# Optimization experiments

Measured on AMD Instinct MI355X. Metric: run time of the kernel, lower is better.

## Reference

```python
import jax, jax.numpy as jnp
import numpy as np


def conv1d(x, w, b, pad):
    # x: (B, Cin, T), w: (Cout, Cin, K), b: (Cout,)
    y = jax.lax.conv_general_dilated(x, w, window_strides=(1,), padding=[(pad, pad)],
                                     dimension_numbers=('NCH', 'OIH', 'NCH'))
    return y + b[None, :, None]


def setup_inputs() -> dict:
    key = jax.random.key(0)
    ks = jax.random.split(key, 16)
    B, Cmel, Ctxt, Catt, T1, T2 = 16, 80, 256, 80, 800, 200
    s = 0.05
    return {
        'queries': jax.random.normal(ks[0], (B, Cmel, T1), jnp.float32),
        'keys': jax.random.normal(ks[1], (B, Ctxt, T2), jnp.float32),
        'attn_prior': jax.random.uniform(ks[2], (B, T1, T2), jnp.float32),
        # key_proj: Conv1d(256->512,k=3,pad=1) -> ReLU -> Conv1d(512->80,k=1)
        'kw1': jax.random.normal(ks[3], (Ctxt * 2, Ctxt, 3), jnp.float32) * s,
        'kb1': jax.random.normal(ks[4], (Ctxt * 2,), jnp.float32) * s,
        'kw2': jax.random.normal(ks[5], (Catt, Ctxt * 2, 1), jnp.float32) * s,
        'kb2': jax.random.normal(ks[6], (Catt,), jnp.float32) * s,
        # query_proj (3xconv): 80->160 k3 -> ReLU -> 160->80 k1 -> ReLU -> 80->80 k1
        'qw1': jax.random.normal(ks[7], (Cmel * 2, Cmel, 3), jnp.float32) * s,
        'qb1': jax.random.normal(ks[8], (Cmel * 2,), jnp.float32) * s,
        'qw2': jax.random.normal(ks[9], (Cmel, Cmel * 2, 1), jnp.float32) * s,
        'qb2': jax.random.normal(ks[10], (Cmel,), jnp.float32) * s,
        'qw3': jax.random.normal(ks[11], (Catt, Cmel, 1), jnp.float32) * s,
        'qb3': jax.random.normal(ks[12], (Catt,), jnp.float32) * s,
    }


def reference(queries, keys, attn_prior, kw1, kb1, kw2, kb2, qw1, qb1, qw2, qb2, qw3, qb3):
    # key encoder
    k = jax.nn.relu(conv1d(keys, kw1, kb1, pad=1))
    k = conv1d(k, kw2, kb2, pad=0)                      # (B, Catt, T2)
    # query encoder ('3xconv')
    q = jax.nn.relu(conv1d(queries, qw1, qb1, pad=1))
    q = jax.nn.relu(conv1d(q, qw2, qb2, pad=0))
    q = conv1d(q, qw3, qb3, pad=0)                      # (B, Catt, T1)
    # L2 distance over channels: ||q||^2 + ||k||^2 - 2 q.k (same math as broadcast (q-k)^2 sum)
    q2 = jnp.sum(q * q, axis=1)                         # (B, T1)
    k2 = jnp.sum(k * k, axis=1)                         # (B, T2)
    qk = jnp.einsum('bct,bcs->bts', q, k)               # (B, T1, T2)
    attn = -0.0005 * (q2[:, :, None] + k2[:, None, :] - 2.0 * qk)[:, None]  # (B,1,T1,T2)
    attn = jax.nn.log_softmax(attn, axis=3) + jnp.log(attn_prior[:, None] + 1e-8)
    return attn
```

## Files before the change

### kernel.cpp

```cpp
#include <hip/hip_runtime.h>
#include <cstdint>
#include <cmath>

using short8  = __attribute__((ext_vector_type(8))) short;
using short4v = __attribute__((ext_vector_type(4))) short;
using floatx4 = __attribute__((ext_vector_type(4))) float;

__device__ __forceinline__ short f2bf(float f) {
  union { float f; unsigned u; } x; x.f = f;
  unsigned r = x.u + 0x7FFFu + ((x.u >> 16) & 1u);
  return (short)(r >> 16);
}

__global__ __launch_bounds__(256) void prep_kernel(
    const float* __restrict__ keys, const float* __restrict__ queries,
    const float* __restrict__ kw1, const float* __restrict__ kw2,
    const float* __restrict__ qw1, const float* __restrict__ qw2,
    const float* __restrict__ qw3,
    short* __restrict__ kT0, short* __restrict__ qT0,
    short* __restrict__ w1, short* __restrict__ w2, short* __restrict__ w3,
    short* __restrict__ w4, short* __restrict__ w5)
{
  const int bid = blockIdx.x, tid = threadIdx.x;
  __shared__ float xs[32][65];

  if (bid < 1136) {
    const float* src; short* dst; int CIN, T, CP, bx, by, b;
    if (bid < 512) {
      src = keys; dst = kT0; CIN = 256; T = 200; CP = 256;
      bx = bid & 3; by = (bid >> 2) & 7; b = bid >> 5;
    } else {
      int b2 = bid - 512;
      src = queries; dst = qT0; CIN = 80; T = 800; CP = 96;
      bx = b2 % 13; by = (b2 / 13) % 3; b = b2 / 39;
    }
    const int t0 = bx * 64, ci0 = by * 32;
    for (int i = tid; i < 32 * 64; i += 256) {
      int row = i >> 6, col = i & 63;
      float v = 0.f;
      if (ci0 + row < CIN && t0 + col < T)
        v = src[((size_t)b * CIN + ci0 + row) * T + t0 + col];
      xs[row][col] = v;
    }
    __syncthreads();
    int t = tid >> 2, c8 = (tid & 3) * 8;
    if (t0 + t < T) {
      short8 o;
      #pragma unroll
      for (int j = 0; j < 8; ++j) o[j] = f2bf(xs[c8 + j][t]);
      *(short8*)&dst[((size_t)b * T + t0 + t) * CP + ci0 + c8] = o;
    }
  } else {
    int blk = bid - 1136;
    const float* src; short* dst; int base, tot;
    int CoP, CiP, Cout, CIN, K;
    if      (blk < 384) { src=kw1; dst=w1; base=0;   CoP=512; CiP=256; Cout=512; CIN=256; K=3; }
    else if (blk < 432) { src=kw2; dst=w2; base=384; CoP=96;  CiP=512; Cout=80;  CIN=512; K=1; }
    else if (blk < 486) { src=qw1; dst=w3; base=432; CoP=192; CiP=96;  Cout=160; CIN=80;  K=3; }
    else if (blk < 504) { src=qw2; dst=w4; base=486; CoP=96;  CiP=192; Cout=80;  CIN=160; K=1; }
    else                { src=qw3; dst=w5; base=504; CoP=96;  CiP=96;  Cout=80;  CIN=80;  K=1; }
    tot = K * CoP * CiP;
    int b0 = (blk - base) * 1024;
    for (int e = 0; e < 4; ++e) {
      int gi = b0 + e * 256 + tid;
      if (gi < tot) {
        int dk  = gi / (CoP * CiP);
        int rem = gi - dk * (CoP * CiP);
        int co  = rem / CiP, ci = rem - (rem / CiP) * CiP;
        float v = (co < Cout && ci < CIN) ? src[((size_t)co * CIN + ci) * K + dk] : 0.f;
        dst[gi] = f2bf(v);
      }
    }
  }
}

__global__ __launch_bounds__(256) void encoders_kernel(
    const short* __restrict__ kT0, const short* __restrict__ qT0,
    const short* __restrict__ w1, const short* __restrict__ w2,
    const short* __restrict__ w3, const short* __restrict__ w4,
    const short* __restrict__ w5,
    const float* __restrict__ kb1, const float* __restrict__ kb2,
    const float* __restrict__ qb1, const float* __restrict__ qb2,
    const float* __restrict__ qb3,
    short* __restrict__ kF, short* __restrict__ qF)
{
  __shared__ __align__(16) short smem[25680];
  const int tid = threadIdx.x, wid = tid >> 6, lane = tid & 63;
  const int q = lane >> 4, m = lane & 15;
  short* xs = smem;

  if (blockIdx.x < 64) {
    const int b = blockIdx.x >> 2, t0 = (blockIdx.x & 3) * 64;
    short* y1c = smem + 2640;

    floatx4 acc2[6];
    #pragma unroll
    for (int f = 0; f < 6; ++f) acc2[f] = (floatx4){0.f, 0.f, 0.f, 0.f};

    for (int half = 0; half < 2; ++half) {
      floatx4 acc1[4][4];
      #pragma unroll
      for (int f = 0; f < 4; ++f)
        #pragma unroll
        for (int tf = 0; tf < 4; ++tf) acc1[f][tf] = (floatx4){0.f, 0.f, 0.f, 0.f};

      for (int c0 = 0; c0 < 8; ++c0) {
        __syncthreads();
        for (int i = tid; i < 66 * 4; i += 256) {
          int row = i >> 2, c8 = (i & 3) * 8;
          int t = t0 + row - 1;
          int4 v = {0, 0, 0, 0};
          if (t >= 0 && t < 200)
            v = *(const int4*)&kT0[((size_t)b * 200 + t) * 256 + c0 * 32 + c8];
          *(int4*)&xs[row * 40 + c8] = v;
        }
        __syncthreads();
        #pragma unroll
        for (int dk = 0; dk < 3; ++dk) {
          short8 fa[4];
          #pragma unroll
          for (int f = 0; f < 4; ++f)
            fa[f] = *(const short8*)&w1[((size_t)(dk * 512 + half * 256 + wid * 64 + f * 16 + m)) * 256
                                        + c0 * 32 + q * 8];
          #pragma unroll
          for (int tf = 0; tf < 4; ++tf) {
            short8 fb = *(const short8*)&xs[(tf * 16 + m + dk) * 40 + q * 8];
            #pragma unroll
            for (int f = 0; f < 4; ++f)
              acc1[f][tf] = __builtin_amdgcn_mfma_f32_16x16x32_bf16(fa[f], fb, acc1[f][tf], 0, 0, 0);
          }
        }
      }
      __syncthreads();
      #pragma unroll
      for (int f = 0; f < 4; ++f) {
        #pragma unroll
        for (int tf = 0; tf < 4; ++tf) {
          int co_l = wid * 64 + f * 16 + q * 4;
          int co   = half * 256 + co_l;
          int t    = tf * 16 + m;
          short4v o;
          #pragma unroll
          for (int r = 0; r < 4; ++r)
            o[r] = f2bf(fmaxf(acc1[f][tf][r] + kb1[co + r], 0.f));
          *(short4v*)&y1c[(co_l >> 5) * 2560 + t * 40 + (co_l & 31)] = o;
        }
      }
      __syncthreads();
      #pragma unroll
      for (int c = 0; c < 8; ++c) {
        short8 fb = *(const short8*)&y1c[c * 2560 + (wid * 16 + m) * 40 + q * 8];
        #pragma unroll
        for (int f = 0; f < 6; ++f) {
          short8 fa = *(const short8*)&w2[((size_t)(f * 16 + m)) * 512 + half * 256 + c * 32 + q * 8];
          acc2[f] = __builtin_amdgcn_mfma_f32_16x16x32_bf16(fa, fb, acc2[f], 0, 0, 0);
        }
      }
    }
    int t = t0 + wid * 16 + m;
    if (t < 200) {
      #pragma unroll
      for (int f = 0; f < 6; ++f) {
        int co = f * 16 + q * 4;
        short4v o;
        #pragma unroll
        for (int r = 0; r < 4; ++r) {
          float bv = (co + r < 80) ? kb2[co + r] : 0.f;
          o[r] = f2bf(acc2[f][r] + bv);
        }
        *(short4v*)&kF[((size_t)b * 200 + t) * 96 + co] = o;
      }
    }
  } else {
    const int qbid = blockIdx.x - 64;
    const int b = qbid / 13, t0 = (qbid % 13) * 64;
    short* y1c = smem + 2640;
    short* y2c = smem + 18000;

    floatx4 accq[3][4];
    #pragma unroll
    for (int f = 0; f < 3; ++f)
      #pragma unroll
      for (int tf = 0; tf < 4; ++tf) accq[f][tf] = (floatx4){0.f, 0.f, 0.f, 0.f};

    for (int c0 = 0; c0 < 3; ++c0) {
      __syncthreads();
      for (int i = tid; i < 66 * 4; i += 256) {
        int row = i >> 2, c8 = (i & 3) * 8;
        int t = t0 + row - 1;
        int4 v = {0, 0, 0, 0};
        if (t >= 0 && t < 800)
          v = *(const int4*)&qT0[((size_t)b * 800 + t) * 96 + c0 * 32 + c8];
        *(int4*)&xs[row * 40 + c8] = v;
      }
      __syncthreads();
      #pragma unroll
      for (int dk = 0; dk < 3; ++dk) {
        short8 fa[3];
        #pragma unroll
        for (int f = 0; f < 3; ++f)
          fa[f] = *(const short8*)&w3[((size_t)(dk * 192 + wid * 48 + f * 16 + m)) * 96
                                      + c0 * 32 + q * 8];
        #pragma unroll
        for (int tf = 0; tf < 4; ++tf) {
          short8 fb = *(const short8*)&xs[(tf * 16 + m + dk) * 40 + q * 8];
          #pragma unroll
          for (int f = 0; f < 3; ++f)
            accq[f][tf] = __builtin_amdgcn_mfma_f32_16x16x32_bf16(fa[f], fb, accq[f][tf], 0, 0, 0);
        }
      }
    }
    __syncthreads();
    #pragma unroll
    for (int f = 0; f < 3; ++f) {
      #pragma unroll
      for (int tf = 0; tf < 4; ++tf) {
        int co = wid * 48 + f * 16 + q * 4;
        int t  = tf * 16 + m;
        short4v o;
        #pragma unroll
        for (int r = 0; r < 4; ++r) {
          float bv = (co + r < 160) ? qb1[co + r] : 0.f;
          o[r] = f2bf(fmaxf(accq[f][tf][r] + bv, 0.f));
        }
        *(short4v*)&y1c[(co >> 5) * 2560 + t * 40 + (co & 31)] = o;
      }
    }
    __syncthreads();

    floatx4 acc2q[6];
    #pragma unroll
    for (int f = 0; f < 6; ++f) acc2q[f] = (floatx4){0.f, 0.f, 0.f, 0.f};
    #pragma unroll
    for (int c = 0; c < 6; ++c) {
      short8 fb = *(const short8*)&y1c[c * 2560 + (wid * 16 + m) * 40 + q * 8];
      #pragma unroll
      for (int f = 0; f < 6; ++f) {
        short8 fa = *(const short8*)&w4[((size_t)(f * 16 + m)) * 192 + c * 32 + q * 8];
        acc2q[f] = __builtin_amdgcn_mfma_f32_16x16x32_bf16(fa, fb, acc2q[f], 0, 0, 0);
      }
    }
    #pragma unroll
    for (int f = 0; f < 6; ++f) {
      int co = f * 16 + q * 4;
      int t  = wid * 16 + m;
      short4v o;
      #pragma unroll
      for (int r = 0; r < 4; ++r) {
        float bv = (co + r < 80) ? qb2[co + r] : 0.f;
        o[r] = f2bf(fmaxf(acc2q[f][r] + bv, 0.f));
      }
      *(short4v*)&y2c[(co >> 5) * 2560 + t * 40 + (co & 31)] = o;
    }
    __syncthreads();

    floatx4 acc3q[6];
    #pragma unroll
    for (int f = 0; f < 6; ++f) acc3q[f] = (floatx4){0.f, 0.f, 0.f, 0.f};
    #pragma unroll
    for (int c = 0; c < 3; ++c) {
      short8 fb = *(const short8*)&y2c[c * 2560 + (wid * 16 + m) * 40 + q * 8];
      #pragma unroll
      for (int f = 0; f < 6; ++f) {
        short8 fa = *(const short8*)&w5[((size_t)(f * 16 + m)) * 96 + c * 32 + q * 8];
        acc3q[f] = __builtin_amdgcn_mfma_f32_16x16x32_bf16(fa, fb, acc3q[f], 0, 0, 0);
      }
    }
    int t = t0 + wid * 16 + m;
    if (t < 800) {
      #pragma unroll
      for (int f = 0; f < 6; ++f) {
        int co = f * 16 + q * 4;
        short4v o;
        #pragma unroll
        for (int r = 0; r < 4; ++r) {
          float bv = (co + r < 80) ? qb3[co + r] : 0.f;
          o[r] = f2bf(acc3q[f][r] + bv);
        }
        *(short4v*)&qF[((size_t)b * 800 + t) * 96 + co] = o;
      }
    }
  }
}

__global__ __launch_bounds__(256) void attn_mfma(
    const short* __restrict__ qT, const short* __restrict__ kT,
    const float* __restrict__ prior, float* __restrict__ out)
{
  const int b = blockIdx.y, t1_0 = blockIdx.x * 64;
  const int tid = threadIdx.x, wid = tid >> 6, lane = tid & 63;
  const int q = lane >> 4, m = lane & 15;

  __shared__ __align__(16) short aq[64 * 104];
  __shared__ __align__(16) short bk[208 * 40];
  __shared__ float k2s[208];

  floatx4 acc[13];
  #pragma unroll
  for (int f = 0; f < 13; ++f) acc[f] = (floatx4){0.f, 0.f, 0.f, 0.f};

  for (int i = tid; i < 64 * 12; i += 256) {
    int row = i / 12, g = i - (i / 12) * 12;
    int4 v = {0, 0, 0, 0};
    if (t1_0 + row < 800)
      v = *(const int4*)&qT[((size_t)b * 800 + t1_0 + row) * 96 + g * 8];
    *(int4*)&aq[row * 104 + g * 8] = v;
  }

  float k2acc = 0.f;
  for (int c = 0; c < 3; ++c) {
    __syncthreads();
    for (int i = tid; i < 208 * 4; i += 256) {
      int row = i >> 2, g = i & 3;
      int4 v = {0, 0, 0, 0};
      if (row < 200)
        v = *(const int4*)&kT[((size_t)b * 200 + row) * 96 + c * 32 + g * 8];
      *(int4*)&bk[row * 40 + g * 8] = v;
    }
    __syncthreads();
    if (tid < 208) {
      #pragma unroll
      for (int g = 0; g < 4; ++g) {
        short8 s = *(const short8*)&bk[tid * 40 + g * 8];
        #pragma unroll
        for (int j = 0; j < 8; ++j) {
          union { unsigned u; float f; } x; x.u = ((unsigned)(unsigned short)s[j]) << 16;
          k2acc = fmaf(x.f, x.f, k2acc);
        }
      }
    }
    short8 fa = *(const short8*)&aq[(wid * 16 + m) * 104 + c * 32 + q * 8];
    #pragma unroll
    for (int f = 0; f < 13; ++f) {
      short8 fb = *(const short8*)&bk[(f * 16 + m) * 40 + q * 8];
      acc[f] = __builtin_amdgcn_mfma_f32_16x16x32_bf16(fa, fb, acc[f], 0, 0, 0);
    }
  }
  if (tid < 208) k2s[tid] = k2acc;
  __syncthreads();

  float k2v[13];
  #pragma unroll
  for (int f = 0; f < 13; ++f) k2v[f] = k2s[f * 16 + m];

  float mx[4] = {-INFINITY, -INFINITY, -INFINITY, -INFINITY};
  #pragma unroll
  for (int f = 0; f < 13; ++f) {
    bool valid = (f * 16 + m) < 200;
    #pragma unroll
    for (int r = 0; r < 4; ++r) {
      float v = valid ? (0.001f * acc[f][r] - 0.0005f * k2v[f]) : -INFINITY;
      acc[f][r] = v;
      mx[r] = fmaxf(mx[r], v);
    }
  }
  #pragma unroll
  for (int msk = 1; msk < 16; msk <<= 1)
    #pragma unroll
    for (int r = 0; r < 4; ++r) mx[r] = fmaxf(mx[r], __shfl_xor(mx[r], msk));
  float sm[4] = {0.f, 0.f, 0.f, 0.f};
  #pragma unroll
  for (int f = 0; f < 13; ++f)
    #pragma unroll
    for (int r = 0; r < 4; ++r) sm[r] += __expf(acc[f][r] - mx[r]);
  #pragma unroll
  for (int msk = 1; msk < 16; msk <<= 1)
    #pragma unroll
    for (int r = 0; r < 4; ++r) sm[r] += __shfl_xor(sm[r], msk);
  float lse[4];
  #pragma unroll
  for (int r = 0; r < 4; ++r) lse[r] = mx[r] + __logf(sm[r]);

  #pragma unroll
  for (int f = 0; f < 13; ++f) {
    int col = f * 16 + m;
    if (col < 200) {
      #pragma unroll
      for (int r = 0; r < 4; ++r) {
        int t1 = t1_0 + wid * 16 + q * 4 + r;
        if (t1 < 800) {
          size_t o = ((size_t)b * 800 + t1) * 200 + col;
          out[o] = acc[f][r] - lse[r] + __logf(prior[o] + 1e-8f);
        }
      }
    }
  }
}

extern "C" void kernel_launch(void* const* d_in, const int* in_sizes, int n_in,
                              void* d_out, int out_size, void* d_ws, size_t ws_size,
                              hipStream_t stream) {
  const float* queries = (const float*)d_in[0];
  const float* keys    = (const float*)d_in[1];
  const float* prior   = (const float*)d_in[2];
  const float* kw1 = (const float*)d_in[3];
  const float* kb1 = (const float*)d_in[4];
  const float* kw2 = (const float*)d_in[5];
  const float* kb2 = (const float*)d_in[6];
  const float* qw1 = (const float*)d_in[7];
  const float* qb1 = (const float*)d_in[8];
  const float* qw2 = (const float*)d_in[9];
  const float* qb2 = (const float*)d_in[10];
  const float* qw3 = (const float*)d_in[11];
  const float* qb3 = (const float*)d_in[12];
  float* out = (float*)d_out;

  short* p = (short*)d_ws;
  short* kT0 = p;  p += (size_t)3200 * 256;
  short* qT0 = p;  p += (size_t)12800 * 96;
  short* w1  = p;  p += (size_t)3 * 512 * 256;
  short* w2  = p;  p += (size_t)96 * 512;
  short* w3  = p;  p += (size_t)3 * 192 * 96;
  short* w4  = p;  p += (size_t)96 * 192;
  short* w5  = p;  p += (size_t)96 * 96;
  short* kF  = p;  p += (size_t)3200 * 96;
  short* qF  = p;  p += (size_t)12800 * 96;

  prep_kernel<<<dim3(1649), 256, 0, stream>>>(keys, queries, kw1, kw2, qw1, qw2, qw3,
                                              kT0, qT0, w1, w2, w3, w4, w5);
  encoders_kernel<<<dim3(272), 256, 0, stream>>>(kT0, qT0, w1, w2, w3, w4, w5,
                                                 kb1, kb2, qb1, qb2, qb3, kF, qF);
  attn_mfma<<<dim3(13, 16), 256, 0, stream>>>(qF, kF, prior, out);
}
```

Baseline: 169.5 us.

## Split fused key encoder into parallel k3 conv blocks plus separate 1x1 conv kernel

The key-encoder path previously ran on only 64 blocks, each computing all 512 conv1 output channels and then the 1x1 conv, which serialized heavy MFMA work on few CUs. It is now split so that 512 blocks each compute a 64-channel by 64-time tile of the k=3 conv, with weights staged in LDS. The intermediate is written to a new global bf16 buffer, and a separate 64-block kernel performs the 512->80 projection. This trades extra global traffic and a kernel launch for far more parallelism across the GPU.

```diff
diff --git a/kernel.cpp b/kernel.cpp
--- a/kernel.cpp
+++ b/kernel.cpp
@@ -52,14 +52,14 @@
     }
   } else {
     int blk = bid - 1136;
-    const float* src; short* dst; int base, tot;
+    const float* src; short* dst; int base;
     int CoP, CiP, Cout, CIN, K;
     if      (blk < 384) { src=kw1; dst=w1; base=0;   CoP=512; CiP=256; Cout=512; CIN=256; K=3; }
     else if (blk < 432) { src=kw2; dst=w2; base=384; CoP=96;  CiP=512; Cout=80;  CIN=512; K=1; }
     else if (blk < 486) { src=qw1; dst=w3; base=432; CoP=192; CiP=96;  Cout=160; CIN=80;  K=3; }
     else if (blk < 504) { src=qw2; dst=w4; base=486; CoP=96;  CiP=192; Cout=80;  CIN=160; K=1; }
     else                { src=qw3; dst=w5; base=504; CoP=96;  CiP=96;  Cout=80;  CIN=80;  K=1; }
-    tot = K * CoP * CiP;
+    int tot = K * CoP * CiP;
     int b0 = (blk - base) * 1024;
     for (int e = 0; e < 4; ++e) {
       int gi = b0 + e * 256 + tid;
@@ -74,105 +74,77 @@
   }
 }
 
-__global__ __launch_bounds__(256) void encoders_kernel(
+__global__ __launch_bounds__(256) void conv_k3_kernel(
     const short* __restrict__ kT0, const short* __restrict__ qT0,
-    const short* __restrict__ w1, const short* __restrict__ w2,
-    const short* __restrict__ w3, const short* __restrict__ w4,
-    const short* __restrict__ w5,
-    const float* __restrict__ kb1, const float* __restrict__ kb2,
-    const float* __restrict__ qb1, const float* __restrict__ qb2,
-    const float* __restrict__ qb3,
-    short* __restrict__ kF, short* __restrict__ qF)
+    const short* __restrict__ w1, const short* __restrict__ w3,
+    const short* __restrict__ w4, const short* __restrict__ w5,
+    const float* __restrict__ kb1, const float* __restrict__ qb1,
+    const float* __restrict__ qb2, const float* __restrict__ qb3,
+    short* __restrict__ kT1, short* __restrict__ qF)
 {
   __shared__ __align__(16) short smem[25680];
   const int tid = threadIdx.x, wid = tid >> 6, lane = tid & 63;
   const int q = lane >> 4, m = lane & 15;
   short* xs = smem;
 
-  if (blockIdx.x < 64) {
-    const int b = blockIdx.x >> 2, t0 = (blockIdx.x & 3) * 64;
-    short* y1c = smem + 2640;
-
-    floatx4 acc2[6];
-    #pragma unroll
-    for (int f = 0; f < 6; ++f) acc2[f] = (floatx4){0.f, 0.f, 0.f, 0.f};
-
-    for (int half = 0; half < 2; ++half) {
-      floatx4 acc1[4][4];
-      #pragma unroll
-      for (int f = 0; f < 4; ++f)
-        #pragma unroll
-        for (int tf = 0; tf < 4; ++tf) acc1[f][tf] = (floatx4){0.f, 0.f, 0.f, 0.f};
-
-      for (int c0 = 0; c0 < 8; ++c0) {
-        __syncthreads();
-        for (int i = tid; i < 66 * 4; i += 256) {
-          int row = i >> 2, c8 = (i & 3) * 8;
-          int t = t0 + row - 1;
-          int4 v = {0, 0, 0, 0};
-          if (t >= 0 && t < 200)
-            v = *(const int4*)&kT0[((size_t)b * 200 + t) * 256 + c0 * 32 + c8];
-          *(int4*)&xs[row * 40 + c8] = v;
-        }
-        __syncthreads();
-        #pragma unroll
-        for (int dk = 0; dk < 3; ++dk) {
-          short8 fa[4];
-          #pragma unroll
-          for (int f = 0; f < 4; ++f)
-            fa[f] = *(const short8*)&w1[((size_t)(dk * 512 + half * 256 + wid * 64 + f * 16 + m)) * 256
-                                        + c0 * 32 + q * 8];
-          #pragma unroll
-          for (int tf = 0; tf < 4; ++tf) {
-            short8 fb = *(const short8*)&xs[(tf * 16 + m + dk) * 40 + q * 8];
-            #pragma unroll
-            for (int f = 0; f < 4; ++f)
-              acc1[f][tf] = __builtin_amdgcn_mfma_f32_16x16x32_bf16(fa[f], fb, acc1[f][tf], 0, 0, 0);
+  if (blockIdx.x < 512) {
+    const int blk = blockIdx.x;
+    const int b = blk >> 5, co0 = ((blk >> 2) & 7) * 64, t0 = (blk & 3) * 64;
+    const int wy = wid >> 1, wx = wid & 1;
+    short* as = smem + 2640;
+
+    floatx4 acc[2][2];
+    #pragma unroll
+    for (int i = 0; i < 2; ++i)
+      #pragma unroll
+      for (int j = 0; j < 2; ++j) acc[i][j] = (floatx4){0.f, 0.f, 0.f, 0.f};
+
+    for (int c0 = 0; c0 < 8; ++c0) {
+      __syncthreads();
+      for (int i = tid; i < 66 * 4; i += 256) {
+        int row = i >> 2, c8 = (i & 3) * 8;
+        int t = t0 + row - 1;
+        int4 v = {0, 0, 0, 0};
+        if (t >= 0 && t < 200)
+          v = *(const int4*)&kT0[((size_t)b * 200 + t) * 256 + c0 * 32 + c8];
+        *(int4*)&xs[row * 40 + c8] = v;
+      }
+      for (int i = tid; i < 192 * 4; i += 256) {
+        int row = i >> 2, c8 = (i & 3) * 8;
+        int dk = row >> 6, co = row & 63;
+        *(int4*)&as[row * 40 + c8] =
+            *(const int4*)&w1[((size_t)(dk * 512 + co0 + co)) * 256 + c0 * 32 + c8];
+      }
+      __syncthreads();
+      #pragma unroll
+      for (int dk = 0; dk < 3; ++dk) {
+        short8 fa0 = *(const short8*)&as[(dk * 64 + wy * 32 + m) * 40 + q * 8];
+        short8 fa1 = *(const short8*)&as[(dk * 64 + wy * 32 + 16 + m) * 40 + q * 8];
+        #pragma unroll
+        for (int j = 0; j < 2; ++j) {
+          short8 fb = *(const short8*)&xs[(wx * 32 + j * 16 + m + dk) * 40 + q * 8];
+          acc[0][j] = __builtin_amdgcn_mfma_f32_16x16x32_bf16(fa0, fb, acc[0][j], 0, 0, 0);
+          acc[1][j] = __builtin_amdgcn_mfma_f32_16x16x32_bf16(fa1, fb, acc[1][j], 0, 0, 0);
+        }
+      }
+    }
+    #pragma unroll
+    for (int i = 0; i < 2; ++i) {
+      #pragma unroll
+      for (int j = 0; j < 2; ++j) {
+        #pragma unroll
+        for (int r = 0; r < 4; ++r) {
+          int co = co0 + wy * 32 + i * 16 + q * 4 + r;
+          int t  = t0 + wx * 32 + j * 16 + m;
+          if (t < 200) {
+            float v = fmaxf(acc[i][j][r] + kb1[co], 0.f);
+            kT1[((size_t)b * 200 + t) * 512 + co] = f2bf(v);
           }
         }
       }
-      __syncthreads();
-      #pragma unroll
-      for (int f = 0; f < 4; ++f) {
-        #pragma unroll
-        for (int tf = 0; tf < 4; ++tf) {
-          int co_l = wid * 64 + f * 16 + q * 4;
-          int co   = half * 256 + co_l;
-          int t    = tf * 16 + m;
-          short4v o;
-          #pragma unroll
-          for (int r = 0; r < 4; ++r)
-            o[r] = f2bf(fmaxf(acc1[f][tf][r] + kb1[co + r], 0.f));
-          *(short4v*)&y1c[(co_l >> 5) * 2560 + t * 40 + (co_l & 31)] = o;
-        }
-      }
-      __syncthreads();
-      #pragma unroll
-      for (int c = 0; c < 8; ++c) {
-        short8 fb = *(const short8*)&y1c[c * 2560 + (wid * 16 + m) * 40 + q * 8];
-        #pragma unroll
-        for (int f = 0; f < 6; ++f) {
-          short8 fa = *(const short8*)&w2[((size_t)(f * 16 + m)) * 512 + half * 256 + c * 32 + q * 8];
-          acc2[f] = __builtin_amdgcn_mfma_f32_16x16x32_bf16(fa, fb, acc2[f], 0, 0, 0);
-        }
-      }
-    }
-    int t = t0 + wid * 16 + m;
-    if (t < 200) {
-      #pragma unroll
-      for (int f = 0; f < 6; ++f) {
-        int co = f * 16 + q * 4;
-        short4v o;
-        #pragma unroll
-        for (int r = 0; r < 4; ++r) {
-          float bv = (co + r < 80) ? kb2[co + r] : 0.f;
-          o[r] = f2bf(acc2[f][r] + bv);
-        }
-        *(short4v*)&kF[((size_t)b * 200 + t) * 96 + co] = o;
-      }
     }
   } else {
-    const int qbid = blockIdx.x - 64;
+    const int qbid = blockIdx.x - 512;
     const int b = qbid / 13, t0 = (qbid % 13) * 64;
     short* y1c = smem + 2640;
     short* y2c = smem + 18000;
@@ -279,6 +251,47 @@
         }
         *(short4v*)&qF[((size_t)b * 800 + t) * 96 + co] = o;
       }
+    }
+  }
+}
+
+__global__ __launch_bounds__(256) void kconv2_kernel(
+    const short* __restrict__ kT1, const short* __restrict__ w2,
+    const float* __restrict__ kb2, short* __restrict__ kF)
+{
+  const int blk = blockIdx.x;
+  const int b = blk >> 2, t0 = (blk & 3) * 64;
+  const int tid = threadIdx.x, wid = tid >> 6, lane = tid & 63;
+  const int q = lane >> 4, m = lane & 15;
+  const int t = t0 + wid * 16 + m;
+  const bool tv = (t < 200);
+
+  floatx4 acc[6];
+  #pragma unroll
+  for (int f = 0; f < 6; ++f) acc[f] = (floatx4){0.f, 0.f, 0.f, 0.f};
+
+  #pragma unroll
+  for (int c = 0; c < 16; ++c) {
+    short8 fb;
+    if (tv) fb = *(const short8*)&kT1[((size_t)b * 200 + t) * 512 + c * 32 + q * 8];
+    else    fb = (short8){0,0,0,0,0,0,0,0};
+    #pragma unroll
+    for (int f = 0; f < 6; ++f) {
+      short8 fa = *(const short8*)&w2[((size_t)(f * 16 + m)) * 512 + c * 32 + q * 8];
+      acc[f] = __builtin_amdgcn_mfma_f32_16x16x32_bf16(fa, fb, acc[f], 0, 0, 0);
+    }
+  }
+  if (tv) {
+    #pragma unroll
+    for (int f = 0; f < 6; ++f) {
+      int co = f * 16 + q * 4;
+      short4v o;
+      #pragma unroll
+      for (int r = 0; r < 4; ++r) {
+        float bv = (co + r < 80) ? kb2[co + r] : 0.f;
+        o[r] = f2bf(acc[f][r] + bv);
+      }
+      *(short4v*)&kF[((size_t)b * 200 + t) * 96 + co] = o;
     }
   }
 }
@@ -413,12 +426,14 @@
   short* w3  = p;  p += (size_t)3 * 192 * 96;
   short* w4  = p;  p += (size_t)96 * 192;
   short* w5  = p;  p += (size_t)96 * 96;
+  short* kT1 = p;  p += (size_t)3200 * 512;
   short* kF  = p;  p += (size_t)3200 * 96;
   short* qF  = p;  p += (size_t)12800 * 96;
 
   prep_kernel<<<dim3(1649), 256, 0, stream>>>(keys, queries, kw1, kw2, qw1, qw2, qw3,
                                               kT0, qT0, w1, w2, w3, w4, w5);
-  encoders_kernel<<<dim3(272), 256, 0, stream>>>(kT0, qT0, w1, w2, w3, w4, w5,
-                                                 kb1, kb2, qb1, qb2, qb3, kF, qF);
+  conv_k3_kernel<<<dim3(720), 256, 0, stream>>>(kT0, qT0, w1, w3, w4, w5,
+                                                kb1, qb1, qb2, qb3, kT1, qF);
+  kconv2_kernel<<<dim3(64), 256, 0, stream>>>(kT1, w2, kb2, kF);
   attn_mfma<<<dim3(13, 16), 256, 0, stream>>>(qF, kF, prior, out);
 }
```

Measured after the change: 152.7 us. 1.11x faster.

## Fuse input transpose/bf16 conversion into encoders and retile key encoder

Applied to the files above, without the earlier changes.

Removes the separate activation transpose-and-convert pass from the prep kernel; the encoder kernel now reads fp32 keys/queries directly, converts them to bf16 into shared memory, and loads the whole channel range once instead of per channel chunk. The key encoder is retiled to 16 timesteps per block over all 512 output channels (208 blocks instead of 64), which raises parallelism but re-reads the conv weights per block. The attention kernel now stages all key channels at once and computes k² in a single pass, cutting the barriers inside its loop. Uncoalesced strided global reads of fp32 inputs during staging are a possible cost.

```diff
diff --git a/kernel.cpp b/kernel.cpp
--- a/kernel.cpp
+++ b/kernel.cpp
@@ -13,69 +13,36 @@
 }
 
 __global__ __launch_bounds__(256) void prep_kernel(
-    const float* __restrict__ keys, const float* __restrict__ queries,
     const float* __restrict__ kw1, const float* __restrict__ kw2,
     const float* __restrict__ qw1, const float* __restrict__ qw2,
     const float* __restrict__ qw3,
-    short* __restrict__ kT0, short* __restrict__ qT0,
     short* __restrict__ w1, short* __restrict__ w2, short* __restrict__ w3,
     short* __restrict__ w4, short* __restrict__ w5)
 {
-  const int bid = blockIdx.x, tid = threadIdx.x;
-  __shared__ float xs[32][65];
-
-  if (bid < 1136) {
-    const float* src; short* dst; int CIN, T, CP, bx, by, b;
-    if (bid < 512) {
-      src = keys; dst = kT0; CIN = 256; T = 200; CP = 256;
-      bx = bid & 3; by = (bid >> 2) & 7; b = bid >> 5;
-    } else {
-      int b2 = bid - 512;
-      src = queries; dst = qT0; CIN = 80; T = 800; CP = 96;
-      bx = b2 % 13; by = (b2 / 13) % 3; b = b2 / 39;
-    }
-    const int t0 = bx * 64, ci0 = by * 32;
-    for (int i = tid; i < 32 * 64; i += 256) {
-      int row = i >> 6, col = i & 63;
-      float v = 0.f;
-      if (ci0 + row < CIN && t0 + col < T)
-        v = src[((size_t)b * CIN + ci0 + row) * T + t0 + col];
-      xs[row][col] = v;
-    }
-    __syncthreads();
-    int t = tid >> 2, c8 = (tid & 3) * 8;
-    if (t0 + t < T) {
-      short8 o;
-      #pragma unroll
-      for (int j = 0; j < 8; ++j) o[j] = f2bf(xs[c8 + j][t]);
-      *(short8*)&dst[((size_t)b * T + t0 + t) * CP + ci0 + c8] = o;
-    }
-  } else {
-    int blk = bid - 1136;
-    const float* src; short* dst; int base, tot;
-    int CoP, CiP, Cout, CIN, K;
-    if      (blk < 384) { src=kw1; dst=w1; base=0;   CoP=512; CiP=256; Cout=512; CIN=256; K=3; }
-    else if (blk < 432) { src=kw2; dst=w2; base=384; CoP=96;  CiP=512; Cout=80;  CIN=512; K=1; }
-    else if (blk < 486) { src=qw1; dst=w3; base=432; CoP=192; CiP=96;  Cout=160; CIN=80;  K=3; }
-    else if (blk < 504) { src=qw2; dst=w4; base=486; CoP=96;  CiP=192; Cout=80;  CIN=160; K=1; }
-    else                { src=qw3; dst=w5; base=504; CoP=96;  CiP=96;  Cout=80;  CIN=80;  K=1; }
-    tot = K * CoP * CiP;
-    int b0 = (blk - base) * 1024;
-    for (int e = 0; e < 4; ++e) {
-      int gi = b0 + e * 256 + tid;
-      if (gi < tot) {
-        int dk  = gi / (CoP * CiP);
-        int rem = gi - dk * (CoP * CiP);
-        int co  = rem / CiP, ci = rem - (rem / CiP) * CiP;
-        float v = (co < Cout && ci < CIN) ? src[((size_t)co * CIN + ci) * K + dk] : 0.f;
-        dst[gi] = f2bf(v);
-      }
+  const int blk = blockIdx.x, tid = threadIdx.x;
+  const float* src; short* dst; int base;
+  int CoP, CiP, Cout, CIN, K;
+  if      (blk < 384) { src=kw1; dst=w1; base=0;   CoP=512; CiP=256; Cout=512; CIN=256; K=3; }
+  else if (blk < 432) { src=kw2; dst=w2; base=384; CoP=96;  CiP=512; Cout=80;  CIN=512; K=1; }
+  else if (blk < 486) { src=qw1; dst=w3; base=432; CoP=192; CiP=96;  Cout=160; CIN=80;  K=3; }
+  else if (blk < 504) { src=qw2; dst=w4; base=486; CoP=96;  CiP=192; Cout=80;  CIN=160; K=1; }
+  else                { src=qw3; dst=w5; base=504; CoP=96;  CiP=96;  Cout=80;  CIN=80;  K=1; }
+  int tot = K * CoP * CiP;
+  int b0 = (blk - base) * 1024;
+  for (int e = 0; e < 4; ++e) {
+    int gi = b0 + e * 256 + tid;
+    if (gi < tot) {
+      int dk  = gi / (CoP * CiP);
+      int rem = gi - dk * (CoP * CiP);
+      int co  = rem / CiP, ci = rem - (rem / CiP) * CiP;
+      float v = (co < Cout && ci < CIN) ? src[((size_t)co * CIN + ci) * K + dk] : 0.f;
+      dst[gi] = f2bf(v);
     }
   }
 }
 
 __global__ __launch_bounds__(256) void encoders_kernel(
-    const short* __restrict__ kT0, const short* __restrict__ qT0,
+    const float* __restrict__ keys, const float* __restrict__ queries,
     const short* __restrict__ w1, const short* __restrict__ w2,
     const short* __restrict__ w3, const short* __restrict__ w4,
     const short* __restrict__ w5,
@@ -84,98 +51,100 @@
     const float* __restrict__ qb3,
     short* __restrict__ kF, short* __restrict__ qF)
 {
-  __shared__ __align__(16) short smem[25680];
-  const int tid = threadIdx.x, wid = tid >> 6, lane = tid & 63;
+  __shared__ __align__(16) short smem[22224];
+  const int tid = threadIdx.x, wv = tid >> 6, lane = tid & 63;
   const int q = lane >> 4, m = lane & 15;
-  short* xs = smem;
-
-  if (blockIdx.x < 64) {
-    const int b = blockIdx.x >> 2, t0 = (blockIdx.x & 3) * 64;
-    short* y1c = smem + 2640;
-
-    floatx4 acc2[6];
-    #pragma unroll
-    for (int f = 0; f < 6; ++f) acc2[f] = (floatx4){0.f, 0.f, 0.f, 0.f};
-
-    for (int half = 0; half < 2; ++half) {
-      floatx4 acc1[4][4];
-      #pragma unroll
-      for (int f = 0; f < 4; ++f)
-        #pragma unroll
-        for (int tf = 0; tf < 4; ++tf) acc1[f][tf] = (floatx4){0.f, 0.f, 0.f, 0.f};
-
-      for (int c0 = 0; c0 < 8; ++c0) {
-        __syncthreads();
-        for (int i = tid; i < 66 * 4; i += 256) {
-          int row = i >> 2, c8 = (i & 3) * 8;
-          int t = t0 + row - 1;
-          int4 v = {0, 0, 0, 0};
-          if (t >= 0 && t < 200)
-            v = *(const int4*)&kT0[((size_t)b * 200 + t) * 256 + c0 * 32 + c8];
-          *(int4*)&xs[row * 40 + c8] = v;
-        }
-        __syncthreads();
-        #pragma unroll
-        for (int dk = 0; dk < 3; ++dk) {
-          short8 fa[4];
-          #pragma unroll
-          for (int f = 0; f < 4; ++f)
-            fa[f] = *(const short8*)&w1[((size_t)(dk * 512 + half * 256 + wid * 64 + f * 16 + m)) * 256
-                                        + c0 * 32 + q * 8];
-          #pragma unroll
-          for (int tf = 0; tf < 4; ++tf) {
-            short8 fb = *(const short8*)&xs[(tf * 16 + m + dk) * 40 + q * 8];
-            #pragma unroll
-            for (int f = 0; f < 4; ++f)
-              acc1[f][tf] = __builtin_amdgcn_mfma_f32_16x16x32_bf16(fa[f], fb, acc1[f][tf], 0, 0, 0);
-          }
-        }
-      }
-      __syncthreads();
-      #pragma unroll
-      for (int f = 0; f < 4; ++f) {
-        #pragma unroll
-        for (int tf = 0; tf < 4; ++tf) {
-          int co_l = wid * 64 + f * 16 + q * 4;
-          int co   = half * 256 + co_l;
-          int t    = tf * 16 + m;
-          short4v o;
-          #pragma unroll
-          for (int r = 0; r < 4; ++r)
-            o[r] = f2bf(fmaxf(acc1[f][tf][r] + kb1[co + r], 0.f));
-          *(short4v*)&y1c[(co_l >> 5) * 2560 + t * 40 + (co_l & 31)] = o;
-        }
-      }
-      __syncthreads();
-      #pragma unroll
-      for (int c = 0; c < 8; ++c) {
-        short8 fb = *(const short8*)&y1c[c * 2560 + (wid * 16 + m) * 40 + q * 8];
-        #pragma unroll
-        for (int f = 0; f < 6; ++f) {
-          short8 fa = *(const short8*)&w2[((size_t)(f * 16 + m)) * 512 + half * 256 + c * 32 + q * 8];
-          acc2[f] = __builtin_amdgcn_mfma_f32_16x16x32_bf16(fa, fb, acc2[f], 0, 0, 0);
-        }
-      }
-    }
-    int t = t0 + wid * 16 + m;
+
+  if (blockIdx.x < 208) {
+    const int b = blockIdx.x / 13, t0 = (blockIdx.x % 13) * 16;
+    short* xs = smem;
+    short* y1 = smem + 4752;
+
+    {
+      const int ci = tid;
+      #pragma unroll
+      for (int j = 0; j < 18; ++j) {
+        int t = t0 - 1 + j;
+        float v = (t >= 0 && t < 200) ? keys[((size_t)b * 256 + ci) * 200 + t] : 0.f;
+        xs[j * 264 + ci] = f2bf(v);
+      }
+    }
+    __syncthreads();
+
+    floatx4 acc1[8];
+    #pragma unroll
+    for (int f = 0; f < 8; ++f) acc1[f] = (floatx4){0.f, 0.f, 0.f, 0.f};
+
+    for (int c0 = 0; c0 < 8; ++c0) {
+      #pragma unroll
+      for (int dk = 0; dk < 3; ++dk) {
+        short8 fb = *(const short8*)&xs[(m + dk) * 264 + c0 * 32 + q * 8];
+        #pragma unroll
+        for (int f = 0; f < 8; ++f) {
+          short8 fa = *(const short8*)&w1[(size_t)dk * 131072
+                                          + (wv * 128 + f * 16 + m) * 256 + c0 * 32 + q * 8];
+          acc1[f] = __builtin_amdgcn_mfma_f32_16x16x32_bf16(fa, fb, acc1[f], 0, 0, 0);
+        }
+      }
+    }
+    #pragma unroll
+    for (int f = 0; f < 8; ++f) {
+      int co = wv * 128 + f * 16 + q * 4;
+      floatx4 bv = *(const floatx4*)&kb1[co];
+      short4v o;
+      #pragma unroll
+      for (int r = 0; r < 4; ++r) o[r] = f2bf(fmaxf(acc1[f][r] + bv[r], 0.f));
+      *(short4v*)&y1[m * 520 + co] = o;
+    }
+    __syncthreads();
+
+    const int nf = (wv < 2) ? 2 : 1;
+    floatx4 acc2[2];
+    acc2[0] = (floatx4){0.f, 0.f, 0.f, 0.f};
+    acc2[1] = (floatx4){0.f, 0.f, 0.f, 0.f};
+    for (int c0 = 0; c0 < 16; ++c0) {
+      short8 fb = *(const short8*)&y1[m * 520 + c0 * 32 + q * 8];
+      short8 fa0 = *(const short8*)&w2[(wv * 16 + m) * 512 + c0 * 32 + q * 8];
+      acc2[0] = __builtin_amdgcn_mfma_f32_16x16x32_bf16(fa0, fb, acc2[0], 0, 0, 0);
+      if (nf == 2) {
+        short8 fa1 = *(const short8*)&w2[((wv + 4) * 16 + m) * 512 + c0 * 32 + q * 8];
+        acc2[1] = __builtin_amdgcn_mfma_f32_16x16x32_bf16(fa1, fb, acc2[1], 0, 0, 0);
+      }
+    }
+    int t = t0 + m;
     if (t < 200) {
-      #pragma unroll
-      for (int f = 0; f < 6; ++f) {
+      for (int e = 0; e < nf; ++e) {
+        int f = wv + e * 4;
         int co = f * 16 + q * 4;
+        floatx4 bv = {0.f, 0.f, 0.f, 0.f};
+        if (co < 80) bv = *(const floatx4*)&kb2[co];
         short4v o;
         #pragma unroll
-        for (int r = 0; r < 4; ++r) {
-          float bv = (co + r < 80) ? kb2[co + r] : 0.f;
-          o[r] = f2bf(acc2[f][r] + bv);
-        }
+        for (int r = 0; r < 4; ++r) o[r] = f2bf(acc2[e][r] + bv[r]);
         *(short4v*)&kF[((size_t)b * 200 + t) * 96 + co] = o;
       }
     }
   } else {
-    const int qbid = blockIdx.x - 64;
-    const int b = qbid / 13, t0 = (qbid % 13) * 64;
-    short* y1c = smem + 2640;
-    short* y2c = smem + 18000;
+    const int qb = blockIdx.x - 208;
+    const int b = qb / 13, t0 = (qb % 13) * 64;
+    short* xs  = smem;
+    short* y1c = smem + 6864;
+    short* y2c = y1c;
+
+    for (int i = tid; i < 384; i += 256) {
+      int ci = i >> 2, jq = i & 3;
+      #pragma unroll
+      for (int jj = 0; jj < 17; ++jj) {
+        int j = jq * 17 + jj;
+        if (j < 66) {
+          int t = t0 - 1 + j;
+          float v = (ci < 80 && t >= 0 && t < 800)
+                      ? queries[((size_t)b * 80 + ci) * 800 + t] : 0.f;
+          xs[j * 104 + ci] = f2bf(v);
+        }
+      }
+    }
+    __syncthreads();
 
     floatx4 accq[3][4];
     #pragma unroll
@@ -184,26 +153,16 @@
       for (int tf = 0; tf < 4; ++tf) accq[f][tf] = (floatx4){0.f, 0.f, 0.f, 0.f};
 
     for (int c0 = 0; c0 < 3; ++c0) {
-      __syncthreads();
-      for (int i = tid; i < 66 * 4; i += 256) {
-        int row = i >> 2, c8 = (i & 3) * 8;
-        int t = t0 + row - 1;
-        int4 v = {0, 0, 0, 0};
-        if (t >= 0 && t < 800)
-          v = *(const int4*)&qT0[((size_t)b * 800 + t) * 96 + c0 * 32 + c8];
-        *(int4*)&xs[row * 40 + c8] = v;
-      }
-      __syncthreads();
       #pragma unroll
       for (int dk = 0; dk < 3; ++dk) {
         short8 fa[3];
         #pragma unroll
         for (int f = 0; f < 3; ++f)
-          fa[f] = *(const short8*)&w3[((size_t)(dk * 192 + wid * 48 + f * 16 + m)) * 96
+          fa[f] = *(const short8*)&w3[((size_t)(dk * 192 + wv * 48 + f * 16 + m)) * 96
                                       + c0 * 32 + q * 8];
         #pragma unroll
         for (int tf = 0; tf < 4; ++tf) {
-          short8 fb = *(const short8*)&xs[(tf * 16 + m + dk) * 40 + q * 8];
+          short8 fb = *(const short8*)&xs[(tf * 16 + m + dk) * 104 + c0 * 32 + q * 8];
           #pragma unroll
           for (int f = 0; f < 3; ++f)
             accq[f][tf] = __builtin_amdgcn_mfma_f32_16x16x32_bf16(fa[f], fb, accq[f][tf], 0, 0, 0);
@@ -215,7 +174,7 @@
     for (int f = 0; f < 3; ++f) {
       #pragma unroll
       for (int tf = 0; tf < 4; ++tf) {
-        int co = wid * 48 + f * 16 + q * 4;
+        int co = wv * 48 + f * 16 + q * 4;
         int t  = tf * 16 + m;
         short4v o;
         #pragma unroll
@@ -233,17 +192,18 @@
     for (int f = 0; f < 6; ++f) acc2q[f] = (floatx4){0.f, 0.f, 0.f, 0.f};
     #pragma unroll
     for (int c = 0; c < 6; ++c) {
-      short8 fb = *(const short8*)&y1c[c * 2560 + (wid * 16 + m) * 40 + q * 8];
+      short8 fb = *(const short8*)&y1c[c * 2560 + (wv * 16 + m) * 40 + q * 8];
       #pragma unroll
       for (int f = 0; f < 6; ++f) {
         short8 fa = *(const short8*)&w4[((size_t)(f * 16 + m)) * 192 + c * 32 + q * 8];
         acc2q[f] = __builtin_amdgcn_mfma_f32_16x16x32_bf16(fa, fb, acc2q[f], 0, 0, 0);
       }
     }
+    __syncthreads();
     #pragma unroll
     for (int f = 0; f < 6; ++f) {
       int co = f * 16 + q * 4;
-      int t  = wid * 16 + m;
+      int t  = wv * 16 + m;
       short4v o;
       #pragma unroll
       for (int r = 0; r < 4; ++r) {
@@ -259,14 +219,14 @@
     for (int f = 0; f < 6; ++f) acc3q[f] = (floatx4){0.f, 0.f, 0.f, 0.f};
     #pragma unroll
     for (int c = 0; c < 3; ++c) {
-      short8 fb = *(const short8*)&y2c[c * 2560 + (wid * 16 + m) * 40 + q * 8];
+      short8 fb = *(const short8*)&y2c[c * 2560 + (wv * 16 + m) * 40 + q * 8];
       #pragma unroll
       for (int f = 0; f < 6; ++f) {
         short8 fa = *(const short8*)&w5[((size_t)(f * 16 + m)) * 96 + c * 32 + q * 8];
         acc3q[f] = __builtin_amdgcn_mfma_f32_16x16x32_bf16(fa, fb, acc3q[f], 0, 0, 0);
       }
     }
-    int t = t0 + wid * 16 + m;
+    int t = t0 + wv * 16 + m;
     if (t < 800) {
       #pragma unroll
       for (int f = 0; f < 6; ++f) {
@@ -292,12 +252,8 @@
   const int q = lane >> 4, m = lane & 15;
 
   __shared__ __align__(16) short aq[64 * 104];
-  __shared__ __align__(16) short bk[208 * 40];
+  __shared__ __align__(16) short bk[208 * 104];
   __shared__ float k2s[208];
-
-  floatx4 acc[13];
-  #pragma unroll
-  for (int f = 0; f < 13; ++f) acc[f] = (floatx4){0.f, 0.f, 0.f, 0.f};
 
   for (int i = tid; i < 64 * 12; i += 256) {
     int row = i / 12, g = i - (i / 12) * 12;
@@ -306,37 +262,42 @@
       v = *(const int4*)&qT[((size_t)b * 800 + t1_0 + row) * 96 + g * 8];
     *(int4*)&aq[row * 104 + g * 8] = v;
   }
-
-  float k2acc = 0.f;
+  for (int i = tid; i < 208 * 12; i += 256) {
+    int row = i / 12, g = i - (i / 12) * 12;
+    int4 v = {0, 0, 0, 0};
+    if (row < 200)
+      v = *(const int4*)&kT[((size_t)b * 200 + row) * 96 + g * 8];
+    *(int4*)&bk[row * 104 + g * 8] = v;
+  }
+  __syncthreads();
+
+  if (tid < 208) {
+    float k2acc = 0.f;
+    #pragma unroll
+    for (int g = 0; g < 12; ++g) {
+      short8 s = *(const short8*)&bk[tid * 104 + g * 8];
+      #pragma unroll
+      for (int j = 0; j < 8; ++j) {
+        union { unsigned u; float f; } x; x.u = ((unsigned)(unsigned short)s[j]) << 16;
+        k2acc = fmaf(x.f, x.f, k2acc);
+      }
+    }
+    k2s[tid] = k2acc;
+  }
+
+  floatx4 acc[13];
+  #pragma unroll
+  for (int f = 0; f < 13; ++f) acc[f] = (floatx4){0.f, 0.f, 0.f, 0.f};
+
+  #pragma unroll
   for (int c = 0; c < 3; ++c) {
-    __syncthreads();
-    for (int i = tid; i < 208 * 4; i += 256) {
-      int row = i >> 2, g = i & 3;
-      int4 v = {0, 0, 0, 0};
-      if (row < 200)
-        v = *(const int4*)&kT[((size_t)b * 200 + row) * 96 + c * 32 + g * 8];
-      *(int4*)&bk[row * 40 + g * 8] = v;
-    }
-    __syncthreads();
-    if (tid < 208) {
-      #pragma unroll
-      for (int g = 0; g < 4; ++g) {
-        short8 s = *(const short8*)&bk[tid * 40 + g * 8];
-        #pragma unroll
-        for (int j = 0; j < 8; ++j) {
-          union { unsigned u; float f; } x; x.u = ((unsigned)(unsigned short)s[j]) << 16;
-          k2acc = fmaf(x.f, x.f, k2acc);
-        }
-      }
-    }
     short8 fa = *(const short8*)&aq[(wid * 16 + m) * 104 + c * 32 + q * 8];
     #pragma unroll
     for (int f = 0; f < 13; ++f) {
-      short8 fb = *(const short8*)&bk[(f * 16 + m) * 40 + q * 8];
+      short8 fb = *(const short8*)&bk[(f * 16 + m) * 104 + c * 32 + q * 8];
       acc[f] = __builtin_amdgcn_mfma_f32_16x16x32_bf16(fa, fb, acc[f], 0, 0, 0);
     }
   }
-  if (tid < 208) k2s[tid] = k2acc;
   __syncthreads();
 
   float k2v[13];
@@ -406,19 +367,17 @@
   float* out = (float*)d_out;
 
   short* p = (short*)d_ws;
-  short* kT0 = p;  p += (size_t)3200 * 256;
-  short* qT0 = p;  p += (size_t)12800 * 96;
-  short* w1  = p;  p += (size_t)3 * 512 * 256;
-  short* w2  = p;  p += (size_t)96 * 512;
-  short* w3  = p;  p += (size_t)3 * 192 * 96;
-  short* w4  = p;  p += (size_t)96 * 192;
-  short* w5  = p;  p += (size_t)96 * 96;
-  short* kF  = p;  p += (size_t)3200 * 96;
-  short* qF  = p;  p += (size_t)12800 * 96;
-
-  prep_kernel<<<dim3(1649), 256, 0, stream>>>(keys, queries, kw1, kw2, qw1, qw2, qw3,
-                                              kT0, qT0, w1, w2, w3, w4, w5);
-  encoders_kernel<<<dim3(272), 256, 0, stream>>>(kT0, qT0, w1, w2, w3, w4, w5,
+  short* w1 = p;  p += (size_t)3 * 512 * 256;
+  short* w2 = p;  p += (size_t)96 * 512;
+  short* w3 = p;  p += (size_t)3 * 192 * 96;
+  short* w4 = p;  p += (size_t)96 * 192;
+  short* w5 = p;  p += (size_t)96 * 96;
+  short* kF = p;  p += (size_t)3200 * 96;
+  short* qF = p;  p += (size_t)12800 * 96;
+
+  prep_kernel<<<dim3(513), 256, 0, stream>>>(kw1, kw2, qw1, qw2, qw3,
+                                             w1, w2, w3, w4, w5);
+  encoders_kernel<<<dim3(416), 256, 0, stream>>>(keys, queries, w1, w2, w3, w4, w5,
                                                  kb1, kb2, qb1, qb2, qb3, kF, qF);
   attn_mfma<<<dim3(13, 16), 256, 0, stream>>>(qF, kF, prior, out);
 }
```

Result: faster. 155.8 us (-8.1%).
